# Kernel optimization log

Hardware: AMD Instinct MI355X
Metric: run time of the kernel (lower is better)

Reference implementation:

```python
import jax, jax.numpy as jnp
import numpy as np

W_BITS = 4
A_BITS = 8
D_IN = 2048
D_OUT = 2048
B, S = 4, 4096


def _random_hadamard(n, seed=0):
    # Sylvester construction (n must be a power of two), random sign flip, orthonormal scaling
    H = np.array([[1.0]], dtype=np.float64)
    while H.shape[0] < n:
        H = np.block([[H, H], [H, -H]])
    rng = np.random.RandomState(seed)
    signs = np.where(rng.rand(n) < 0.5, -1.0, 1.0)
    return ((H * signs[None, :]) / np.sqrt(n)).astype(np.float32)


def weight_fake_quant(w, bits):
    # GPTQ-style per-output-channel symmetric fake quantization
    maxq = float(2 ** bits - 1)
    zeros = jnp.zeros((w.shape[0], 1), w.dtype)
    xmin = jnp.minimum(w.min(axis=1, keepdims=True), zeros)
    xmax = jnp.maximum(w.max(axis=1, keepdims=True), zeros)
    xmax = jnp.maximum(jnp.abs(xmin), xmax)
    xmin = jnp.where(xmin < 0, -xmax, xmin)
    degen = (xmin == 0) & (xmax == 0)
    xmin = jnp.where(degen, -1.0, xmin)
    xmax = jnp.where(degen, 1.0, xmax)
    scale = (xmax - xmin) / maxq
    zero = (maxq + 1.0) / 2.0
    q = jnp.clip(jnp.round(w / scale) + zero, 0.0, maxq)
    return scale * (q - zero)


def act_fake_quant(x, bits):
    # per-token symmetric fake quantization (a_groupsize = -1)
    qmax = float(2 ** (bits - 1) - 1)
    s = jnp.max(jnp.abs(x), axis=-1, keepdims=True) / qmax
    s = jnp.maximum(s, 1e-8)
    return jnp.clip(jnp.round(x / s), -(qmax + 1.0), qmax) * s


def setup_inputs() -> dict:
    key = jax.random.key(0)
    k1, k2, k3 = jax.random.split(key, 3)
    hidden_states = jax.random.normal(k1, (B, S, D_IN), dtype=jnp.float32)
    weight = jax.random.normal(k2, (D_OUT, D_IN), dtype=jnp.float32) * 0.02
    bias = jax.random.normal(k3, (D_OUT,), dtype=jnp.float32) * 0.02
    rotation_matrix = jnp.asarray(_random_hadamard(D_IN))
    channel_wise_scale = jnp.ones((1, D_IN), dtype=jnp.float32)
    clip_factor_w_max = jnp.ones((D_OUT, 1), dtype=jnp.float32) * 4.0
    clip_factor_w_min = jnp.ones((D_OUT, 1), dtype=jnp.float32) * 4.0
    return {
        "hidden_states": hidden_states,
        "weight": weight,
        "bias": bias,
        "rotation_matrix": rotation_matrix,
        "channel_wise_scale": channel_wise_scale,
        "clip_factor_w_max": clip_factor_w_max,
        "clip_factor_w_min": clip_factor_w_min,
    }


def reference(hidden_states, weight, bias, rotation_matrix, channel_wise_scale,
              clip_factor_w_max, clip_factor_w_min):
    # _train_forward path: rotate -> smooth -> lwc clip -> weight fake-quant,
    # rotate -> smooth -> act fake-quant -> linear
    w = jnp.matmul(weight, rotation_matrix)          # [O, I]
    w = w * channel_wise_scale                        # smooth scale [1, I]
    wmin = w.min(axis=1, keepdims=True) * jax.nn.sigmoid(clip_factor_w_min)
    wmax = w.max(axis=1, keepdims=True) * jax.nn.sigmoid(clip_factor_w_max)
    w = jnp.clip(w, wmin, wmax)
    w = weight_fake_quant(w, W_BITS)

    h = jnp.matmul(hidden_states, rotation_matrix)    # [B, S, I]
    h = h / channel_wise_scale
    h = act_fake_quant(h, A_BITS)

    out = jnp.einsum("bsi,oi->bso", h, w) + bias      # [B, S, O]
    return out
```

## Files before the change

kernel.cpp:

```cpp
#include <hip/hip_runtime.h>
#include <hip/hip_bf16.h>

#define DIN 2048
#define DOUT 2048
#define NTOK 16384

typedef __bf16 bf16x8 __attribute__((ext_vector_type(8)));
typedef float f32x4 __attribute__((ext_vector_type(4)));
typedef int   i32x4 __attribute__((ext_vector_type(4)));
typedef char  i8x4  __attribute__((ext_vector_type(4)));

__device__ __forceinline__ void load_lds16(const void* g, void* l) {
  __builtin_amdgcn_global_load_lds((const __attribute__((address_space(1))) void*)g,
                                   (__attribute__((address_space(3))) void*)l,
                                   16, 0, 0);
}

__device__ __forceinline__ void store1(float* p, float v) { *p = v; }
__device__ __forceinline__ void store1(__hip_bfloat16* p, float v) { *p = __float2bfloat16(v); }

__device__ __forceinline__ int xcd_swz(int bid, int nwg) {
  const int cpx = nwg >> 3;
  return (bid & 7) * cpx + (bid >> 3);
}

template <typename OutT>
__global__ __launch_bounds__(256) void gemm_bt(
    const __hip_bfloat16* __restrict__ A,
    const __hip_bfloat16* __restrict__ B,
    OutT* __restrict__ C,
    const float* __restrict__ colf,
    int M, int N, int K)
{
  constexpr int BK = 32;
  __shared__ __hip_bfloat16 lA[128 * BK];
  __shared__ __hip_bfloat16 lB[128 * BK];
  const int t = threadIdx.x;
  const int lane = t & 63;
  const int wid = t >> 6;
  const int wr = wid >> 1, wc = wid & 1;
  const int nbn = N / 128;
  const int bid = xcd_swz(blockIdx.x, gridDim.x);
  const long m0 = (long)(bid / nbn) * 128;
  const long n0 = (long)(bid % nbn) * 128;

  const int offB = t * 16;
  const int row0 = offB >> 6;
  const int cole = (offB & 63) >> 1;

  const __hip_bfloat16* gA0 = A + (m0 + row0) * (long)K + cole;
  const __hip_bfloat16* gA1 = gA0 + 64L * K;
  const __hip_bfloat16* gB0 = B + (n0 + row0) * (long)K + cole;
  const __hip_bfloat16* gB1 = gB0 + 64L * K;
  __hip_bfloat16* lAp = lA + t * 8;
  __hip_bfloat16* lBp = lB + t * 8;

  f32x4 acc[4][4] = {};

  const int kr = (lane >> 4) * 8;
  const int rA = wr * 64 + (lane & 15);
  const int rB = wc * 64 + (lane & 15);

  for (int k0 = 0; k0 < K; k0 += BK) {
    __syncthreads();
    load_lds16(gA0 + k0, lAp);
    load_lds16(gA1 + k0, lAp + 2048);
    load_lds16(gB0 + k0, lBp);
    load_lds16(gB1 + k0, lBp + 2048);
    __syncthreads();
    bf16x8 af[4], bfr[4];
#pragma unroll
    for (int m = 0; m < 4; ++m)
      af[m] = *(const bf16x8*)(lA + (rA + m * 16) * BK + kr);
#pragma unroll
    for (int n = 0; n < 4; ++n)
      bfr[n] = *(const bf16x8*)(lB + (rB + n * 16) * BK + kr);
#pragma unroll
    for (int m = 0; m < 4; ++m)
#pragma unroll
      for (int n = 0; n < 4; ++n)
        acc[m][n] = __builtin_amdgcn_mfma_f32_16x16x32_bf16(af[m], bfr[n], acc[m][n], 0, 0, 0);
  }

  const int cr = (lane >> 4) * 4;
  const int cc = lane & 15;
#pragma unroll
  for (int m = 0; m < 4; ++m) {
    const long r0 = m0 + wr * 64 + m * 16 + cr;
#pragma unroll
    for (int n = 0; n < 4; ++n) {
      const long col = n0 + wc * 64 + n * 16 + cc;
      const float f = colf[col];
#pragma unroll
      for (int e = 0; e < 4; ++e)
        store1(&C[(r0 + e) * N + col], acc[m][n][e] * f);
    }
  }
}

__global__ __launch_bounds__(256) void gemm_wsplit2(
    const __hip_bfloat16* __restrict__ Ahi, const __hip_bfloat16* __restrict__ Alo,
    const __hip_bfloat16* __restrict__ Bs,
    float* __restrict__ C,
    const float* __restrict__ colf,
    int M, int N, int K)
{
  constexpr int BK = 32;
  __shared__ __hip_bfloat16 lAhi[128 * BK];
  __shared__ __hip_bfloat16 lAlo[128 * BK];
  __shared__ __hip_bfloat16 lB[64 * BK];
  const int t = threadIdx.x;
  const int lane = t & 63;
  const int wid = t >> 6;
  const int wr = wid >> 1, wc = wid & 1;
  const int nbn = N / 64;
  const int bid = xcd_swz(blockIdx.x, gridDim.x);
  const long m0 = (long)(bid / nbn) * 128;
  const long n0 = (long)(bid % nbn) * 64;

  const int offB = t * 16;
  const int row0 = offB >> 6;
  const int cole = (offB & 63) >> 1;

  const long aoff = (m0 + row0) * (long)K + cole;
  const long boff = (n0 + row0) * (long)K + cole;

  f32x4 acc[4][2] = {};

  const int kr = (lane >> 4) * 8;
  const int rA = wr * 64 + (lane & 15);
  const int rB = wc * 32 + (lane & 15);

  for (int k0 = 0; k0 < K; k0 += BK) {
    __syncthreads();
    load_lds16(Ahi + aoff + k0, lAhi + t * 8);
    load_lds16(Ahi + aoff + 64L * K + k0, lAhi + t * 8 + 2048);
    load_lds16(Alo + aoff + k0, lAlo + t * 8);
    load_lds16(Alo + aoff + 64L * K + k0, lAlo + t * 8 + 2048);
    load_lds16(Bs + boff + k0, lB + t * 8);
    __syncthreads();
    bf16x8 ah[4], al[4], bs[2];
#pragma unroll
    for (int m = 0; m < 4; ++m) {
      ah[m] = *(const bf16x8*)(lAhi + (rA + m * 16) * BK + kr);
      al[m] = *(const bf16x8*)(lAlo + (rA + m * 16) * BK + kr);
    }
#pragma unroll
    for (int n = 0; n < 2; ++n)
      bs[n] = *(const bf16x8*)(lB + (rB + n * 16) * BK + kr);
#pragma unroll
    for (int m = 0; m < 4; ++m)
#pragma unroll
      for (int n = 0; n < 2; ++n) {
        acc[m][n] = __builtin_amdgcn_mfma_f32_16x16x32_bf16(ah[m], bs[n], acc[m][n], 0, 0, 0);
        acc[m][n] = __builtin_amdgcn_mfma_f32_16x16x32_bf16(al[m], bs[n], acc[m][n], 0, 0, 0);
      }
  }

  const int cr = (lane >> 4) * 4;
  const int cc = lane & 15;
#pragma unroll
  for (int m = 0; m < 4; ++m) {
    const long r0 = m0 + wr * 64 + m * 16 + cr;
#pragma unroll
    for (int n = 0; n < 2; ++n) {
      const long col = n0 + wc * 32 + n * 16 + cc;
      const float f = colf[col];
#pragma unroll
      for (int e = 0; e < 4; ++e)
        C[(r0 + e) * N + col] = acc[m][n][e] * f;
    }
  }
}

__global__ __launch_bounds__(256) void gemm_out_i8(
    const char* __restrict__ A,
    const char* __restrict__ B,
    float* __restrict__ C,
    const float* __restrict__ srow,
    const float* __restrict__ wscale,
    const float* __restrict__ bias,
    int M, int N, int K)
{
  constexpr int BK = 64;
  __shared__ char lA[128 * BK];
  __shared__ char lB[128 * BK];
  const int t = threadIdx.x;
  const int lane = t & 63;
  const int wid = t >> 6;
  const int wr = wid >> 1, wc = wid & 1;
  const int nbn = N / 128;
  const int bid = xcd_swz(blockIdx.x, gridDim.x);
  const long m0 = (long)(bid / nbn) * 128;
  const long n0 = (long)(bid % nbn) * 128;

  const int offB = t * 16;
  const int row0 = offB >> 6;
  const int colB = offB & 63;

  const char* gA0 = A + (m0 + row0) * (long)K + colB;
  const char* gA1 = gA0 + 64L * K;
  const char* gB0 = B + (n0 + row0) * (long)K + colB;
  const char* gB1 = gB0 + 64L * K;
  char* lAp = lA + t * 16;
  char* lBp = lB + t * 16;

  i32x4 acc[4][4] = {};

  const int kr16 = (lane >> 4) * 16;
  const int rA = wr * 64 + (lane & 15);
  const int rB = wc * 64 + (lane & 15);

  for (int k0 = 0; k0 < K; k0 += BK) {
    __syncthreads();
    load_lds16(gA0 + k0, lAp);
    load_lds16(gA1 + k0, lAp + 4096);
    load_lds16(gB0 + k0, lBp);
    load_lds16(gB1 + k0, lBp + 4096);
    __syncthreads();
    i32x4 af[4], bfr[4];
#pragma unroll
    for (int m = 0; m < 4; ++m)
      af[m] = *(const i32x4*)(lA + (rA + m * 16) * BK + kr16);
#pragma unroll
    for (int n = 0; n < 4; ++n)
      bfr[n] = *(const i32x4*)(lB + (rB + n * 16) * BK + kr16);
#pragma unroll
    for (int m = 0; m < 4; ++m)
#pragma unroll
      for (int n = 0; n < 4; ++n)
        acc[m][n] = __builtin_amdgcn_mfma_i32_16x16x64_i8(af[m], bfr[n], acc[m][n], 0, 0, 0);
  }

  const int cr = (lane >> 4) * 4;
  const int cc = lane & 15;
#pragma unroll
  for (int m = 0; m < 4; ++m) {
    const long r0 = m0 + wr * 64 + m * 16 + cr;
    const float s0 = srow[r0], s1 = srow[r0 + 1], s2 = srow[r0 + 2], s3 = srow[r0 + 3];
#pragma unroll
    for (int n = 0; n < 4; ++n) {
      const long col = n0 + wc * 64 + n * 16 + cc;
      const float wsC = wscale[col];
      const float bC = bias[col];
      float* o = C + r0 * N + col;
      o[0]      = (float)acc[m][n][0] * (s0 * wsC) + bC;
      o[N]      = (float)acc[m][n][1] * (s1 * wsC) + bC;
      o[2L * N] = (float)acc[m][n][2] * (s2 * wsC) + bC;
      o[3L * N] = (float)acc[m][n][3] * (s3 * wsC) + bC;
    }
  }
}

__global__ __launch_bounds__(256) void cvt_bf16(const float* __restrict__ in,
                                                __hip_bfloat16* __restrict__ out, int n4)
{
  const int i = blockIdx.x * 256 + threadIdx.x;
  if (i >= n4) return;
  f32x4 v = ((const f32x4*)in)[i];
  __hip_bfloat16 o[4];
#pragma unroll
  for (int j = 0; j < 4; ++j) o[j] = __float2bfloat16(v[j]);
  *(ushort4*)(out + i * 4L) = *(ushort4*)o;
}

__global__ __launch_bounds__(256) void cvt_split(const float* __restrict__ in,
                                                 __hip_bfloat16* __restrict__ hi,
                                                 __hip_bfloat16* __restrict__ lo, int n4)
{
  const int i = blockIdx.x * 256 + threadIdx.x;
  if (i >= n4) return;
  f32x4 v = ((const f32x4*)in)[i];
  __hip_bfloat16 oh[4], ol[4];
#pragma unroll
  for (int j = 0; j < 4; ++j) {
    oh[j] = __float2bfloat16(v[j]);
    ol[j] = __float2bfloat16(v[j] - __bfloat162float(oh[j]));
  }
  *(ushort4*)(hi + i * 4L) = *(ushort4*)oh;
  *(ushort4*)(lo + i * 4L) = *(ushort4*)ol;
}

__global__ __launch_bounds__(256) void transpose_sign(const float* __restrict__ in,
                                                      __hip_bfloat16* __restrict__ out, int N)
{
  __shared__ float tile[32][33];
  const int nb = N >> 5;
  const int bx = blockIdx.x % nb, by = blockIdx.x / nb;
  const int tx = threadIdx.x & 31, ty = threadIdx.x >> 5;
#pragma unroll
  for (int i = 0; i < 4; ++i)
    tile[ty + i * 8][tx] = in[(long)(by * 32 + ty + i * 8) * N + bx * 32 + tx];
  __syncthreads();
#pragma unroll
  for (int i = 0; i < 4; ++i) {
    const float v = tile[tx][ty + i * 8];
    const unsigned short s = (unsigned short)(0x3F80u | ((__float_as_uint(v) >> 16) & 0x8000u));
    *(unsigned short*)&out[(long)(bx * 32 + ty + i * 8) * N + by * 32 + tx] = s;
  }
}

__global__ __launch_bounds__(256) void make_colf(const float* __restrict__ cws,
                                                 const float* __restrict__ R,
                                                 float* __restrict__ colf1,
                                                 float* __restrict__ colf2, int n)
{
  const int i = blockIdx.x * 256 + threadIdx.x;
  const float r0 = fabsf(R[0]);
  if (i < n) {
    colf1[i] = cws[i] * r0;
    colf2[i] = r0 / cws[i];
  }
}

__global__ __launch_bounds__(256) void wquant(
    const float* __restrict__ wrot,
    const float* __restrict__ cfmax, const float* __restrict__ cfmin,
    char* __restrict__ qw, float* __restrict__ wscale)
{
  const int row = blockIdx.x;
  const float* w = wrot + (long)row * DIN;
  const int t = threadIdx.x;
  f32x4 v0 = ((const f32x4*)w)[t];
  f32x4 v1 = ((const f32x4*)w)[t + 256];
  float vmin = v0[0], vmax = v0[0];
#pragma unroll
  for (int j = 1; j < 4; ++j) { vmin = fminf(vmin, v0[j]); vmax = fmaxf(vmax, v0[j]); }
#pragma unroll
  for (int j = 0; j < 4; ++j) { vmin = fminf(vmin, v1[j]); vmax = fmaxf(vmax, v1[j]); }
#pragma unroll
  for (int off = 32; off; off >>= 1) {
    vmin = fminf(vmin, __shfl_xor(vmin, off));
    vmax = fmaxf(vmax, __shfl_xor(vmax, off));
  }
  __shared__ float smin[4], smax[4];
  const int lane = t & 63, wid = t >> 6;
  if (lane == 0) { smin[wid] = vmin; smax[wid] = vmax; }
  __syncthreads();
  vmin = fminf(fminf(smin[0], smin[1]), fminf(smin[2], smin[3]));
  vmax = fmaxf(fmaxf(smax[0], smax[1]), fmaxf(smax[2], smax[3]));

  const float sgmax = 1.f / (1.f + expf(-cfmax[row]));
  const float sgmin = 1.f / (1.f + expf(-cfmin[row]));
  const float wminc = vmin * sgmin;
  const float wmaxc = vmax * sgmax;
  float cmin = fminf(fmaxf(vmin, wminc), wmaxc);
  float cmax = fmaxf(fminf(vmax, wmaxc), wminc);
  float xmin = fminf(cmin, 0.f), xmax = fmaxf(cmax, 0.f);
  const float xm = fmaxf(fabsf(xmin), xmax);
  xmin = (xmin < 0.f) ? -xm : xmin;
  xmax = xm;
  if ((xmin == 0.f) && (xmax == 0.f)) { xmin = -1.f; xmax = 1.f; }
  const float scale = (xmax - xmin) / 15.f;
  if (t == 0) wscale[row] = scale;

  char* qr = qw + (long)row * DIN;
  i8x4 o0, o1;
#pragma unroll
  for (int j = 0; j < 4; ++j) {
    float wc = fminf(fmaxf(v0[j], wminc), wmaxc);
    float q = rintf(wc / scale) + 8.f;
    q = fminf(fmaxf(q, 0.f), 15.f);
    o0[j] = (char)(int)(q - 8.f);
    wc = fminf(fmaxf(v1[j], wminc), wmaxc);
    q = rintf(wc / scale) + 8.f;
    q = fminf(fmaxf(q, 0.f), 15.f);
    o1[j] = (char)(int)(q - 8.f);
  }
  *(i8x4*)(qr + t * 4) = o0;
  *(i8x4*)(qr + 1024 + t * 4) = o1;
}

__global__ __launch_bounds__(256) void hquant(
    const __hip_bfloat16* __restrict__ h,
    char* __restrict__ qh,
    float* __restrict__ srow)
{
  const long row = blockIdx.x;
  const __hip_bfloat16* hr = h + row * DIN;
  const int t = threadIdx.x;
  bf16x8 v = *(const bf16x8*)(hr + t * 8);
  float f[8];
  float amax = 0.f;
#pragma unroll
  for (int j = 0; j < 8; ++j) { f[j] = (float)v[j]; amax = fmaxf(amax, fabsf(f[j])); }
#pragma unroll
  for (int off = 32; off; off >>= 1) amax = fmaxf(amax, __shfl_xor(amax, off));
  __shared__ float sm[4];
  const int lane = t & 63, wid = t >> 6;
  if (lane == 0) sm[wid] = amax;
  __syncthreads();
  amax = fmaxf(fmaxf(sm[0], sm[1]), fmaxf(sm[2], sm[3]));
  const float s = fmaxf(amax / 127.f, 1e-8f);
  if (t == 0) srow[row] = s;
  const float is = 1.f / s;

  char o[8];
#pragma unroll
  for (int j = 0; j < 8; ++j) {
    float q = fminf(fmaxf(rintf(f[j] * is), -128.f), 127.f);
    o[j] = (char)(int)q;
  }
  *(uint2*)(qh + row * DIN + t * 8) = *(uint2*)o;
}

extern "C" void kernel_launch(void* const* d_in, const int* in_sizes, int n_in,
                              void* d_out, int out_size, void* d_ws, size_t ws_size,
                              hipStream_t stream)
{
  const float* X     = (const float*)d_in[0];
  const float* W     = (const float*)d_in[1];
  const float* bias  = (const float*)d_in[2];
  const float* R     = (const float*)d_in[3];
  const float* cws   = (const float*)d_in[4];
  const float* cfmax = (const float*)d_in[5];
  const float* cfmin = (const float*)d_in[6];
  float* out = (float*)d_out;

  float*          wrot = (float*)d_out;
  __hip_bfloat16* Wlo  = (__hip_bfloat16*)((char*)d_out + (size_t)DOUT * DIN * 4);
  __hip_bfloat16* h    = (__hip_bfloat16*)d_out;

  char* ws = (char*)d_ws;
  size_t off = 0;
  auto alloc = [&](size_t bytes) -> void* {
    void* p = ws + off;
    off += (bytes + 255) & ~(size_t)255;
    return p;
  };
  __hip_bfloat16* Xb    = (__hip_bfloat16*)alloc((size_t)NTOK * DIN * 2);
  __hip_bfloat16* Sb    = (__hip_bfloat16*)alloc((size_t)DIN * DIN * 2);
  __hip_bfloat16* Whi   = (__hip_bfloat16*)alloc((size_t)DOUT * DIN * 2);
  char*           qh    = (char*)alloc((size_t)NTOK * DIN);
  char*           qw    = (char*)alloc((size_t)DOUT * DIN);
  float*          wsc   = (float*)alloc(DOUT * 4);
  float*          srow  = (float*)alloc(NTOK * 4);
  float*          colf1 = (float*)alloc(DIN * 4);
  float*          colf2 = (float*)alloc(DIN * 4);

  cvt_bf16<<<(NTOK * DIN / 4 + 255) / 256, 256, 0, stream>>>(X, Xb, NTOK * DIN / 4);
  cvt_split<<<(DOUT * DIN / 4 + 255) / 256, 256, 0, stream>>>(W, Whi, Wlo, DOUT * DIN / 4);
  transpose_sign<<<(DIN / 32) * (DIN / 32), 256, 0, stream>>>(R, Sb, DIN);
  make_colf<<<(DIN + 255) / 256, 256, 0, stream>>>(cws, R, colf1, colf2, DIN);

  gemm_wsplit2<<<(DOUT / 128) * (DIN / 64), 256, 0, stream>>>(
      Whi, Wlo, Sb, wrot, colf1, DOUT, DIN, DIN);

  wquant<<<DOUT, 256, 0, stream>>>(wrot, cfmax, cfmin, qw, wsc);

  gemm_bt<__hip_bfloat16><<<(NTOK / 128) * (DIN / 128), 256, 0, stream>>>(
      Xb, Sb, h, colf2, NTOK, DIN, DIN);

  hquant<<<NTOK, 256, 0, stream>>>(h, qh, srow);

  gemm_out_i8<<<(NTOK / 128) * (DOUT / 128), 256, 0, stream>>>(
      qh, qw, out, srow, wsc, bias, NTOK, DOUT, DIN);
}
```

Measured before the change: 621.3 us.

## Double-buffer LDS tiles and prefetch next K-slice in all GEMM kernels

```diff
diff --git a/kernel.cpp b/kernel.cpp
--- a/kernel.cpp
+++ b/kernel.cpp
@@ -33,8 +33,8 @@
     int M, int N, int K)
 {
   constexpr int BK = 32;
-  __shared__ __hip_bfloat16 lA[128 * BK];
-  __shared__ __hip_bfloat16 lB[128 * BK];
+  __shared__ __hip_bfloat16 lA[2][128 * BK];
+  __shared__ __hip_bfloat16 lB[2][128 * BK];
   const int t = threadIdx.x;
   const int lane = t & 63;
   const int wid = t >> 6;
@@ -52,8 +52,6 @@
   const __hip_bfloat16* gA1 = gA0 + 64L * K;
   const __hip_bfloat16* gB0 = B + (n0 + row0) * (long)K + cole;
   const __hip_bfloat16* gB1 = gB0 + 64L * K;
-  __hip_bfloat16* lAp = lA + t * 8;
-  __hip_bfloat16* lBp = lB + t * 8;
 
   f32x4 acc[4][4] = {};
 
@@ -61,25 +59,37 @@
   const int rA = wr * 64 + (lane & 15);
   const int rB = wc * 64 + (lane & 15);
 
+  load_lds16(gA0, lA[0] + t * 8);
+  load_lds16(gA1, lA[0] + t * 8 + 2048);
+  load_lds16(gB0, lB[0] + t * 8);
+  load_lds16(gB1, lB[0] + t * 8 + 2048);
+  __syncthreads();
+
+  int cur = 0;
   for (int k0 = 0; k0 < K; k0 += BK) {
-    __syncthreads();
-    load_lds16(gA0 + k0, lAp);
-    load_lds16(gA1 + k0, lAp + 2048);
-    load_lds16(gB0 + k0, lBp);
-    load_lds16(gB1 + k0, lBp + 2048);
-    __syncthreads();
+    if (k0 + BK < K) {
+      const int nxt = cur ^ 1;
+      load_lds16(gA0 + k0 + BK, lA[nxt] + t * 8);
+      load_lds16(gA1 + k0 + BK, lA[nxt] + t * 8 + 2048);
+      load_lds16(gB0 + k0 + BK, lB[nxt] + t * 8);
+      load_lds16(gB1 + k0 + BK, lB[nxt] + t * 8 + 2048);
+    }
     bf16x8 af[4], bfr[4];
 #pragma unroll
     for (int m = 0; m < 4; ++m)
-      af[m] = *(const bf16x8*)(lA + (rA + m * 16) * BK + kr);
+      af[m] = *(const bf16x8*)(lA[cur] + (rA + m * 16) * BK + kr);
 #pragma unroll
     for (int n = 0; n < 4; ++n)
-      bfr[n] = *(const bf16x8*)(lB + (rB + n * 16) * BK + kr);
+      bfr[n] = *(const bf16x8*)(lB[cur] + (rB + n * 16) * BK + kr);
+    __builtin_amdgcn_s_setprio(1);
 #pragma unroll
     for (int m = 0; m < 4; ++m)
 #pragma unroll
       for (int n = 0; n < 4; ++n)
         acc[m][n] = __builtin_amdgcn_mfma_f32_16x16x32_bf16(af[m], bfr[n], acc[m][n], 0, 0, 0);
+    __builtin_amdgcn_s_setprio(0);
+    __syncthreads();
+    cur ^= 1;
   }
 
   const int cr = (lane >> 4) * 4;
@@ -106,9 +116,9 @@
     int M, int N, int K)
 {
   constexpr int BK = 32;
-  __shared__ __hip_bfloat16 lAhi[128 * BK];
-  __shared__ __hip_bfloat16 lAlo[128 * BK];
-  __shared__ __hip_bfloat16 lB[64 * BK];
+  __shared__ __hip_bfloat16 lAhi[2][128 * BK];
+  __shared__ __hip_bfloat16 lAlo[2][128 * BK];
+  __shared__ __hip_bfloat16 lB[2][64 * BK];
   const int t = threadIdx.x;
   const int lane = t & 63;
   const int wid = t >> 6;
@@ -131,23 +141,33 @@
   const int rA = wr * 64 + (lane & 15);
   const int rB = wc * 32 + (lane & 15);
 
+  load_lds16(Ahi + aoff, lAhi[0] + t * 8);
+  load_lds16(Ahi + aoff + 64L * K, lAhi[0] + t * 8 + 2048);
+  load_lds16(Alo + aoff, lAlo[0] + t * 8);
+  load_lds16(Alo + aoff + 64L * K, lAlo[0] + t * 8 + 2048);
+  load_lds16(Bs + boff, lB[0] + t * 8);
+  __syncthreads();
+
+  int cur = 0;
   for (int k0 = 0; k0 < K; k0 += BK) {
-    __syncthreads();
-    load_lds16(Ahi + aoff + k0, lAhi + t * 8);
-    load_lds16(Ahi + aoff + 64L * K + k0, lAhi + t * 8 + 2048);
-    load_lds16(Alo + aoff + k0, lAlo + t * 8);
-    load_lds16(Alo + aoff + 64L * K + k0, lAlo + t * 8 + 2048);
-    load_lds16(Bs + boff + k0, lB + t * 8);
-    __syncthreads();
+    if (k0 + BK < K) {
+      const int nxt = cur ^ 1;
+      load_lds16(Ahi + aoff + k0 + BK, lAhi[nxt] + t * 8);
+      load_lds16(Ahi + aoff + 64L * K + k0 + BK, lAhi[nxt] + t * 8 + 2048);
+      load_lds16(Alo + aoff + k0 + BK, lAlo[nxt] + t * 8);
+      load_lds16(Alo + aoff + 64L * K + k0 + BK, lAlo[nxt] + t * 8 + 2048);
+      load_lds16(Bs + boff + k0 + BK, lB[nxt] + t * 8);
+    }
     bf16x8 ah[4], al[4], bs[2];
 #pragma unroll
     for (int m = 0; m < 4; ++m) {
-      ah[m] = *(const bf16x8*)(lAhi + (rA + m * 16) * BK + kr);
-      al[m] = *(const bf16x8*)(lAlo + (rA + m * 16) * BK + kr);
+      ah[m] = *(const bf16x8*)(lAhi[cur] + (rA + m * 16) * BK + kr);
+      al[m] = *(const bf16x8*)(lAlo[cur] + (rA + m * 16) * BK + kr);
     }
 #pragma unroll
     for (int n = 0; n < 2; ++n)
-      bs[n] = *(const bf16x8*)(lB + (rB + n * 16) * BK + kr);
+      bs[n] = *(const bf16x8*)(lB[cur] + (rB + n * 16) * BK + kr);
+    __builtin_amdgcn_s_setprio(1);
 #pragma unroll
     for (int m = 0; m < 4; ++m)
 #pragma unroll
@@ -155,6 +175,9 @@
         acc[m][n] = __builtin_amdgcn_mfma_f32_16x16x32_bf16(ah[m], bs[n], acc[m][n], 0, 0, 0);
         acc[m][n] = __builtin_amdgcn_mfma_f32_16x16x32_bf16(al[m], bs[n], acc[m][n], 0, 0, 0);
       }
+    __builtin_amdgcn_s_setprio(0);
+    __syncthreads();
+    cur ^= 1;
   }
 
   const int cr = (lane >> 4) * 4;
@@ -183,8 +206,8 @@
     int M, int N, int K)
 {
   constexpr int BK = 64;
-  __shared__ char lA[128 * BK];
-  __shared__ char lB[128 * BK];
+  __shared__ char lA[2][128 * BK];
+  __shared__ char lB[2][128 * BK];
   const int t = threadIdx.x;
   const int lane = t & 63;
   const int wid = t >> 6;
@@ -202,8 +225,6 @@
   const char* gA1 = gA0 + 64L * K;
   const char* gB0 = B + (n0 + row0) * (long)K + colB;
   const char* gB1 = gB0 + 64L * K;
-  char* lAp = lA + t * 16;
-  char* lBp = lB + t * 16;
 
   i32x4 acc[4][4] = {};
 
@@ -211,25 +232,37 @@
   const int rA = wr * 64 + (lane & 15);
   const int rB = wc * 64 + (lane & 15);
 
+  load_lds16(gA0, lA[0] + t * 16);
+  load_lds16(gA1, lA[0] + t * 16 + 4096);
+  load_lds16(gB0, lB[0] + t * 16);
+  load_lds16(gB1, lB[0] + t * 16 + 4096);
+  __syncthreads();
+
+  int cur = 0;
   for (int k0 = 0; k0 < K; k0 += BK) {
-    __syncthreads();
-    load_lds16(gA0 + k0, lAp);
-    load_lds16(gA1 + k0, lAp + 4096);
-    load_lds16(gB0 + k0, lBp);
-    load_lds16(gB1 + k0, lBp + 4096);
-    __syncthreads();
+    if (k0 + BK < K) {
+      const int nxt = cur ^ 1;
+      load_lds16(gA0 + k0 + BK, lA[nxt] + t * 16);
+      load_lds16(gA1 + k0 + BK, lA[nxt] + t * 16 + 4096);
+      load_lds16(gB0 + k0 + BK, lB[nxt] + t * 16);
+      load_lds16(gB1 + k0 + BK, lB[nxt] + t * 16 + 4096);
+    }
     i32x4 af[4], bfr[4];
 #pragma unroll
     for (int m = 0; m < 4; ++m)
-      af[m] = *(const i32x4*)(lA + (rA + m * 16) * BK + kr16);
+      af[m] = *(const i32x4*)(lA[cur] + (rA + m * 16) * BK + kr16);
 #pragma unroll
     for (int n = 0; n < 4; ++n)
-      bfr[n] = *(const i32x4*)(lB + (rB + n * 16) * BK + kr16);
+      bfr[n] = *(const i32x4*)(lB[cur] + (rB + n * 16) * BK + kr16);
+    __builtin_amdgcn_s_setprio(1);
 #pragma unroll
     for (int m = 0; m < 4; ++m)
 #pragma unroll
       for (int n = 0; n < 4; ++n)
         acc[m][n] = __builtin_amdgcn_mfma_i32_16x16x64_i8(af[m], bfr[n], acc[m][n], 0, 0, 0);
+    __builtin_amdgcn_s_setprio(0);
+    __syncthreads();
+    cur ^= 1;
   }
 
   const int cr = (lane >> 4) * 4;
```

Measured after the change: 593.3 us. 1.05x faster.

## Triple-buffer GEMM K-loops with async LDS prefetch and XOR-swizzled LDS layout

Applied to the files above, without the earlier changes.

```diff
diff --git a/kernel.cpp b/kernel.cpp
--- a/kernel.cpp
+++ b/kernel.cpp
@@ -10,6 +10,12 @@
 typedef int   i32x4 __attribute__((ext_vector_type(4)));
 typedef char  i8x4  __attribute__((ext_vector_type(4)));
 
+#define VMCNT4 asm volatile("s_waitcnt vmcnt(4)" ::: "memory")
+#define VMCNT5 asm volatile("s_waitcnt vmcnt(5)" ::: "memory")
+#define VMCNT0 asm volatile("s_waitcnt vmcnt(0)" ::: "memory")
+#define SCHEDB __builtin_amdgcn_sched_barrier(0)
+#define BARRIER __builtin_amdgcn_s_barrier()
+
 __device__ __forceinline__ void load_lds16(const void* g, void* l) {
   __builtin_amdgcn_global_load_lds((const __attribute__((address_space(1))) void*)g,
                                    (__attribute__((address_space(3))) void*)l,
@@ -22,6 +28,11 @@
 __device__ __forceinline__ int xcd_swz(int bid, int nwg) {
   const int cpx = nwg >> 3;
   return (bid & 7) * cpx + (bid >> 3);
+}
+
+__device__ __forceinline__ int swz_row(int slot) {
+  const int R = slot >> 2;
+  return (R & ~1) | ((R & 1) ^ ((R >> 2) & 1));
 }
 
 template <typename OutT>
@@ -33,8 +44,8 @@
     int M, int N, int K)
 {
   constexpr int BK = 32;
-  __shared__ __hip_bfloat16 lA[128 * BK];
-  __shared__ __hip_bfloat16 lB[128 * BK];
+  constexpr int STRIDE = 16384;
+  __shared__ char lds[3 * STRIDE];
   const int t = threadIdx.x;
   const int lane = t & 63;
   const int wid = t >> 6;
@@ -43,44 +54,65 @@
   const int bid = xcd_swz(blockIdx.x, gridDim.x);
   const long m0 = (long)(bid / nbn) * 128;
   const long n0 = (long)(bid % nbn) * 128;
-
-  const int offB = t * 16;
-  const int row0 = offB >> 6;
-  const int cole = (offB & 63) >> 1;
-
-  const __hip_bfloat16* gA0 = A + (m0 + row0) * (long)K + cole;
+  const int NT = K / BK;
+
+  const int orow = swz_row(t);
+  const int og   = (t & 3) ^ (orow & 3);
+  const int ldst = t * 16;
+
+  const __hip_bfloat16* gA0 = A + (m0 + orow) * (long)K + og * 8;
   const __hip_bfloat16* gA1 = gA0 + 64L * K;
-  const __hip_bfloat16* gB0 = B + (n0 + row0) * (long)K + cole;
+  const __hip_bfloat16* gB0 = B + (n0 + orow) * (long)K + og * 8;
   const __hip_bfloat16* gB1 = gB0 + 64L * K;
-  __hip_bfloat16* lAp = lA + t * 8;
-  __hip_bfloat16* lBp = lB + t * 8;
 
   f32x4 acc[4][4] = {};
 
-  const int kr = (lane >> 4) * 8;
+  const int g16 = (lane >> 4) * 16;
+  const int swzm = (lane & 7) << 4;
   const int rA = wr * 64 + (lane & 15);
   const int rB = wc * 64 + (lane & 15);
-
-  for (int k0 = 0; k0 < K; k0 += BK) {
-    __syncthreads();
-    load_lds16(gA0 + k0, lAp);
-    load_lds16(gA1 + k0, lAp + 2048);
-    load_lds16(gB0 + k0, lBp);
-    load_lds16(gB1 + k0, lBp + 2048);
-    __syncthreads();
+  const int aOff = (rA * 64 + g16) ^ swzm;
+  const int bOff = 8192 + ((rB * 64 + g16) ^ swzm);
+
+  char* pc = lds;
+  char* pn = lds + STRIDE;
+  char* pf = lds + 2 * STRIDE;
+
+#define GBT_ISSUE(buf, kOff)                                   \
+  do {                                                         \
+    load_lds16(gA0 + (kOff), (buf) + ldst);                    \
+    load_lds16(gA1 + (kOff), (buf) + 4096 + ldst);             \
+    load_lds16(gB0 + (kOff), (buf) + 8192 + ldst);             \
+    load_lds16(gB1 + (kOff), (buf) + 8192 + 4096 + ldst);      \
+  } while (0)
+
+  GBT_ISSUE(pc, 0);
+  GBT_ISSUE(pn, BK);
+  VMCNT4; SCHEDB; BARRIER; SCHEDB;
+
+  for (int tt = 0; tt < NT; ++tt) {
+    if (tt + 2 < NT) GBT_ISSUE(pf, (tt + 2) * BK);
     bf16x8 af[4], bfr[4];
 #pragma unroll
     for (int m = 0; m < 4; ++m)
-      af[m] = *(const bf16x8*)(lA + (rA + m * 16) * BK + kr);
+      af[m] = *(const bf16x8*)(pc + aOff + m * 1024);
 #pragma unroll
     for (int n = 0; n < 4; ++n)
-      bfr[n] = *(const bf16x8*)(lB + (rB + n * 16) * BK + kr);
+      bfr[n] = *(const bf16x8*)(pc + bOff + n * 1024);
+    __builtin_amdgcn_s_setprio(1);
 #pragma unroll
     for (int m = 0; m < 4; ++m)
 #pragma unroll
       for (int n = 0; n < 4; ++n)
         acc[m][n] = __builtin_amdgcn_mfma_f32_16x16x32_bf16(af[m], bfr[n], acc[m][n], 0, 0, 0);
-  }
+    __builtin_amdgcn_s_setprio(0);
+    if (tt < NT - 1) {
+      if (tt < NT - 2) { VMCNT4; } else { VMCNT0; }
+      SCHEDB; BARRIER; SCHEDB;
+    }
+    char* tmp = pc; pc = pn; pn = pf; pf = tmp;
+  }
+#undef GBT_ISSUE
 
   const int cr = (lane >> 4) * 4;
   const int cc = lane & 15;
@@ -106,9 +138,8 @@
     int M, int N, int K)
 {
   constexpr int BK = 32;
-  __shared__ __hip_bfloat16 lAhi[128 * BK];
-  __shared__ __hip_bfloat16 lAlo[128 * BK];
-  __shared__ __hip_bfloat16 lB[64 * BK];
+  constexpr int STRIDE = 20480;
+  __shared__ char lds[3 * STRIDE];
   const int t = threadIdx.x;
   const int lane = t & 63;
   const int wid = t >> 6;
@@ -117,37 +148,56 @@
   const int bid = xcd_swz(blockIdx.x, gridDim.x);
   const long m0 = (long)(bid / nbn) * 128;
   const long n0 = (long)(bid % nbn) * 64;
-
-  const int offB = t * 16;
-  const int row0 = offB >> 6;
-  const int cole = (offB & 63) >> 1;
-
-  const long aoff = (m0 + row0) * (long)K + cole;
-  const long boff = (n0 + row0) * (long)K + cole;
+  const int NT = K / BK;
+
+  const int orow = swz_row(t);
+  const int og   = (t & 3) ^ (orow & 3);
+  const int ldst = t * 16;
+
+  const __hip_bfloat16* gH0 = Ahi + (m0 + orow) * (long)K + og * 8;
+  const __hip_bfloat16* gH1 = gH0 + 64L * K;
+  const __hip_bfloat16* gL0 = Alo + (m0 + orow) * (long)K + og * 8;
+  const __hip_bfloat16* gL1 = gL0 + 64L * K;
+  const __hip_bfloat16* gS  = Bs + (n0 + orow) * (long)K + og * 8;
 
   f32x4 acc[4][2] = {};
 
-  const int kr = (lane >> 4) * 8;
+  const int g16 = (lane >> 4) * 16;
+  const int swzm = (lane & 7) << 4;
   const int rA = wr * 64 + (lane & 15);
   const int rB = wc * 32 + (lane & 15);
-
-  for (int k0 = 0; k0 < K; k0 += BK) {
-    __syncthreads();
-    load_lds16(Ahi + aoff + k0, lAhi + t * 8);
-    load_lds16(Ahi + aoff + 64L * K + k0, lAhi + t * 8 + 2048);
-    load_lds16(Alo + aoff + k0, lAlo + t * 8);
-    load_lds16(Alo + aoff + 64L * K + k0, lAlo + t * 8 + 2048);
-    load_lds16(Bs + boff + k0, lB + t * 8);
-    __syncthreads();
+  const int aOff = (rA * 64 + g16) ^ swzm;
+  const int bOff = 16384 + ((rB * 64 + g16) ^ swzm);
+
+  char* pc = lds;
+  char* pn = lds + STRIDE;
+  char* pf = lds + 2 * STRIDE;
+
+#define WSP_ISSUE(buf, kOff)                                    \
+  do {                                                          \
+    load_lds16(gH0 + (kOff), (buf) + ldst);                     \
+    load_lds16(gH1 + (kOff), (buf) + 4096 + ldst);              \
+    load_lds16(gL0 + (kOff), (buf) + 8192 + ldst);              \
+    load_lds16(gL1 + (kOff), (buf) + 8192 + 4096 + ldst);       \
+    load_lds16(gS + (kOff), (buf) + 16384 + ldst);              \
+  } while (0)
+
+  WSP_ISSUE(pc, 0);
+  WSP_ISSUE(pn, BK);
+  VMCNT5; SCHEDB; BARRIER; SCHEDB;
+
+  for (int tt = 0; tt < NT; ++tt) {
+    if (tt + 2 < NT) WSP_ISSUE(pf, (tt + 2) * BK);
     bf16x8 ah[4], al[4], bs[2];
 #pragma unroll
     for (int m = 0; m < 4; ++m) {
-      ah[m] = *(const bf16x8*)(lAhi + (rA + m * 16) * BK + kr);
-      al[m] = *(const bf16x8*)(lAlo + (rA + m * 16) * BK + kr);
+      ah[m] = *(const bf16x8*)(pc + aOff + m * 1024);
+      al[m] = *(const bf16x8*)(pc + 8192 + aOff + m * 1024);
     }
 #pragma unroll
     for (int n = 0; n < 2; ++n)
-      bs[n] = *(const bf16x8*)(lB + (rB + n * 16) * BK + kr);
+      bs[n] = *(const bf16x8*)(pc + bOff + n * 1024);
+    __builtin_amdgcn_s_setprio(1);
 #pragma unroll
     for (int m = 0; m < 4; ++m)
 #pragma unroll
@@ -155,7 +205,14 @@
         acc[m][n] = __builtin_amdgcn_mfma_f32_16x16x32_bf16(ah[m], bs[n], acc[m][n], 0, 0, 0);
         acc[m][n] = __builtin_amdgcn_mfma_f32_16x16x32_bf16(al[m], bs[n], acc[m][n], 0, 0, 0);
       }
-  }
+    __builtin_amdgcn_s_setprio(0);
+    if (tt < NT - 1) {
+      if (tt < NT - 2) { VMCNT5; } else { VMCNT0; }
+      SCHEDB; BARRIER; SCHEDB;
+    }
+    char* tmp = pc; pc = pn; pn = pf; pf = tmp;
+  }
+#undef WSP_ISSUE
 
   const int cr = (lane >> 4) * 4;
   const int cc = lane & 15;
@@ -183,8 +240,8 @@
     int M, int N, int K)
 {
   constexpr int BK = 64;
-  __shared__ char lA[128 * BK];
-  __shared__ char lB[128 * BK];
+  constexpr int STRIDE = 16384;
+  __shared__ char lds[3 * STRIDE];
   const int t = threadIdx.x;
   const int lane = t & 63;
   const int wid = t >> 6;
@@ -193,44 +250,65 @@
   const int bid = xcd_swz(blockIdx.x, gridDim.x);
   const long m0 = (long)(bid / nbn) * 128;
   const long n0 = (long)(bid % nbn) * 128;
-
-  const int offB = t * 16;
-  const int row0 = offB >> 6;
-  const int colB = offB & 63;
-
-  const char* gA0 = A + (m0 + row0) * (long)K + colB;
+  const int NT = K / BK;
+
+  const int orow = swz_row(t);
+  const int og   = (t & 3) ^ (orow & 3);
+  const int ldst = t * 16;
+
+  const char* gA0 = A + (m0 + orow) * (long)K + og * 16;
   const char* gA1 = gA0 + 64L * K;
-  const char* gB0 = B + (n0 + row0) * (long)K + colB;
+  const char* gB0 = B + (n0 + orow) * (long)K + og * 16;
   const char* gB1 = gB0 + 64L * K;
-  char* lAp = lA + t * 16;
-  char* lBp = lB + t * 16;
 
   i32x4 acc[4][4] = {};
 
-  const int kr16 = (lane >> 4) * 16;
+  const int g16 = (lane >> 4) * 16;
+  const int swzm = (lane & 7) << 4;
   const int rA = wr * 64 + (lane & 15);
   const int rB = wc * 64 + (lane & 15);
-
-  for (int k0 = 0; k0 < K; k0 += BK) {
-    __syncthreads();
-    load_lds16(gA0 + k0, lAp);
-    load_lds16(gA1 + k0, lAp + 4096);
-    load_lds16(gB0 + k0, lBp);
-    load_lds16(gB1 + k0, lBp + 4096);
-    __syncthreads();
+  const int aOff = (rA * 64 + g16) ^ swzm;
+  const int bOff = 8192 + ((rB * 64 + g16) ^ swzm);
+
+  char* pc = lds;
+  char* pn = lds + STRIDE;
+  char* pf = lds + 2 * STRIDE;
+
+#define GI8_ISSUE(buf, kOff)                                   \
+  do {                                                         \
+    load_lds16(gA0 + (kOff), (buf) + ldst);                    \
+    load_lds16(gA1 + (kOff), (buf) + 4096 + ldst);             \
+    load_lds16(gB0 + (kOff), (buf) + 8192 + ldst);             \
+    load_lds16(gB1 + (kOff), (buf) + 8192 + 4096 + ldst);      \
+  } while (0)
+
+  GI8_ISSUE(pc, 0);
+  GI8_ISSUE(pn, BK);
+  VMCNT4; SCHEDB; BARRIER; SCHEDB;
+
+  for (int tt = 0; tt < NT; ++tt) {
+    if (tt + 2 < NT) GI8_ISSUE(pf, (tt + 2) * BK);
     i32x4 af[4], bfr[4];
 #pragma unroll
     for (int m = 0; m < 4; ++m)
-      af[m] = *(const i32x4*)(lA + (rA + m * 16) * BK + kr16);
+      af[m] = *(const i32x4*)(pc + aOff + m * 1024);
 #pragma unroll
     for (int n = 0; n < 4; ++n)
-      bfr[n] = *(const i32x4*)(lB + (rB + n * 16) * BK + kr16);
+      bfr[n] = *(const i32x4*)(pc + bOff + n * 1024);
+    __builtin_amdgcn_s_setprio(1);
 #pragma unroll
     for (int m = 0; m < 4; ++m)
 #pragma unroll
       for (int n = 0; n < 4; ++n)
         acc[m][n] = __builtin_amdgcn_mfma_i32_16x16x64_i8(af[m], bfr[n], acc[m][n], 0, 0, 0);
-  }
+    __builtin_amdgcn_s_setprio(0);
+    if (tt < NT - 1) {
+      if (tt < NT - 2) { VMCNT4; } else { VMCNT0; }
+      SCHEDB; BARRIER; SCHEDB;
+    }
+    char* tmp = pc; pc = pn; pn = pf; pf = tmp;
+  }
+#undef GI8_ISSUE
 
   const int cr = (lane >> 4) * 4;
   const int cc = lane & 15;
```

New measurement: 575.7 us. -7.3%, faster.
